# Kernel tuning notes

Measured on AMD Instinct MI355X. Metric: run time of the kernel, lower is better.

The kernel has to match this reference:

```python
import jax, jax.numpy as jnp
import numpy as np

H, NH, NKV, D, I, T, B = 4096, 32, 8, 128, 12288, 1024, 128
THETA, EPS = 1e6, 1e-6


def setup_inputs() -> dict:
    ks = iter(jax.random.split(jax.random.key(0), 64))

    def randn(s):
        return jax.random.normal(next(ks), s, jnp.float32)

    def qw(o, i):
        return jax.random.randint(next(ks), (o, i), 0, 16, jnp.int32)

    def sc(o, g):
        return jax.random.uniform(next(ks), (o, g), jnp.float32, 0.005, 0.02)

    def rot(g):  # block-diagonal rotation, one 128x128 block per input group
        return randn((g, B, B)) / np.float32(np.sqrt(B))

    return dict(
        positions=jnp.arange(T, dtype=jnp.int32),
        hidden_states=randn((T, H)),
        residual=randn((T, H)),
        w_in=jnp.ones(H, jnp.float32), w_post=jnp.ones(H, jnp.float32),
        w_qn=jnp.ones(D, jnp.float32), w_kn=jnp.ones(D, jnp.float32),
        R_q=rot(H // B), qw_q=qw(NH * D, H), sc_q=sc(NH * D, H // B),
        R_k=rot(H // B), qw_k=qw(NKV * D, H), sc_k=sc(NKV * D, H // B),
        R_v=rot(H // B), qw_v=qw(NKV * D, H), sc_v=sc(NKV * D, H // B),
        R_o=rot(NH * D // B), qw_o=qw(H, NH * D), sc_o=sc(H, NH * D // B),
        R_g=rot(H // B), qw_g=qw(I, H), sc_g=sc(I, H // B),
        R_u=rot(H // B), qw_u=qw(I, H), sc_u=sc(I, H // B),
        R_d=rot(I // B), qw_d=qw(H, I), sc_d=sc(H, I // B),
    )


def _rmsnorm(x, w):
    return x * jax.lax.rsqrt(jnp.mean(x * x, -1, keepdims=True) + EPS) * w


def _rot_lin(x, R, qw, sc):
    # RotateLinearInt4: block-rotate input, then int4 group-dequant GEMM.
    G = R.shape[0]
    xr = jnp.einsum('tgi,gij->tgj', x.reshape(-1, G, B), R).reshape(x.shape)
    O = qw.shape[0]
    W = ((qw.astype(x.dtype) - 8.0).reshape(O, G, B) * sc[:, :, None]).reshape(O, G * B)
    return xr @ W.T


def _rope(pos, x):  # neox-style rope, x: [T, h, D]
    half = D // 2
    inv = jnp.power(jnp.float32(THETA), -(jnp.arange(half, dtype=jnp.float32) * (2.0 / D)))
    f = pos.astype(jnp.float32)[:, None] * inv  # [T, half]
    cos, sin = jnp.cos(f)[:, None, :], jnp.sin(f)[:, None, :]
    x1, x2 = x[..., :half], x[..., half:]
    return jnp.concatenate([x1 * cos - x2 * sin, x2 * cos + x1 * sin], -1)


def _forward(positions, hidden_states, residual, w_in, w_post, w_qn, w_kn,
             R_q, qw_q, sc_q, R_k, qw_k, sc_k, R_v, qw_v, sc_v,
             R_o, qw_o, sc_o, R_g, qw_g, sc_g, R_u, qw_u, sc_u,
             R_d, qw_d, sc_d):
    res = hidden_states + residual            # fused add+RMSNorm path
    x = _rmsnorm(res, w_in)
    q = _rot_lin(x, R_q, qw_q, sc_q).reshape(T, NH, D)
    k = _rot_lin(x, R_k, qw_k, sc_k).reshape(T, NKV, D)
    v = _rot_lin(x, R_v, qw_v, sc_v).reshape(T, NKV, D)
    q = _rmsnorm(q, w_qn)                     # per-head q/k RMSNorm
    k = _rmsnorm(k, w_kn)
    q = _rope(positions, q)
    k = _rope(positions, k)
    rep = NH // NKV                           # GQA: repeat kv heads
    kk = jnp.repeat(k, rep, axis=1)
    vv = jnp.repeat(v, rep, axis=1)
    scores = jnp.einsum('thd,shd->hts', q, kk) * (D ** -0.5)
    mask = jnp.tril(jnp.ones((T, T), bool))
    scores = jnp.where(mask, scores, jnp.finfo(scores.dtype).min)
    probs = jax.nn.softmax(scores, -1)
    attn = jnp.einsum('hts,shd->thd', probs, vv).reshape(T, NH * D)
    h = _rot_lin(attn, R_o, qw_o, sc_o)
    res2 = h + res
    x2 = _rmsnorm(res2, w_post)
    gate = _rot_lin(x2, R_g, qw_g, sc_g)
    up = _rot_lin(x2, R_u, qw_u, sc_u)
    h2 = _rot_lin(jax.nn.silu(gate) * up, R_d, qw_d, sc_d)
    return h2, res2


def reference(positions, hidden_states, residual, w_in, w_post, w_qn, w_kn,
              R_q, qw_q, sc_q, R_k, qw_k, sc_k, R_v, qw_v, sc_v,
              R_o, qw_o, sc_o, R_g, qw_g, sc_g, R_u, qw_u, sc_u,
              R_d, qw_d, sc_d):
    return _forward(positions, hidden_states, residual, w_in, w_post, w_qn, w_kn,
                    R_q, qw_q, sc_q, R_k, qw_k, sc_k, R_v, qw_v, sc_v,
                    R_o, qw_o, sc_o, R_g, qw_g, sc_g, R_u, qw_u, sc_u,
                    R_d, qw_d, sc_d)
```

## Files before the change

kernel.cpp:

```cpp
#include <hip/hip_runtime.h>

typedef unsigned short u16;
typedef __attribute__((ext_vector_type(4))) float   f32x4;
typedef __attribute__((ext_vector_type(8))) __bf16  bf16x8;
typedef __attribute__((ext_vector_type(4))) __bf16  bf16x4;
typedef __attribute__((ext_vector_type(8))) short   short8;
typedef __attribute__((ext_vector_type(4))) int     int32x4;
typedef __attribute__((ext_vector_type(4))) short   short4v;

#define MFMA16(a,b,c) __builtin_amdgcn_mfma_f32_16x16x32_bf16(a,b,c,0,0,0)

static __device__ __forceinline__ u16 f2bf(float f){
  unsigned u = __builtin_bit_cast(unsigned, f);
  return (u16)((u + 0x7fffu + ((u >> 16) & 1u)) >> 16);
}
static __device__ __forceinline__ float bf2f(u16 h){
  return __builtin_bit_cast(float, ((unsigned)h) << 16);
}
static __device__ __forceinline__ bf16x8 ldb16(const u16* p){
  return __builtin_bit_cast(bf16x8, *(const short8*)p);
}
static __device__ __forceinline__ void gload_lds16(const void* g, void* l){
  __builtin_amdgcn_global_load_lds(
      reinterpret_cast<const __attribute__((address_space(1))) unsigned int*>(
          reinterpret_cast<unsigned long long>(g)),
      reinterpret_cast<__attribute__((address_space(3))) unsigned int*>(
          reinterpret_cast<unsigned long long>(l)),
      16, 0, 0);
}

static constexpr int T_ = 1024, H_ = 4096, NH_ = 32, NKV_ = 8, I_ = 12288;

__global__ __launch_bounds__(256) void addnorm_kernel(
    const float* __restrict__ a, const float* __restrict__ b,
    const float* __restrict__ w, float* __restrict__ res_out,
    u16* __restrict__ x_out)
{
  const int t = blockIdx.x, tid = threadIdx.x;
  __shared__ float red[4];
  float vals[16]; float ss = 0.f;
  const size_t base = (size_t)t * H_;
  #pragma unroll
  for (int i = 0; i < 16; ++i){
    int c = tid + i*256;
    float v = a[base + c];
    if (b) v += b[base + c];
    vals[i] = v; ss += v*v;
  }
  #pragma unroll
  for (int off = 32; off; off >>= 1) ss += __shfl_xor(ss, off);
  if ((tid & 63) == 0) red[tid >> 6] = ss;
  __syncthreads();
  float tot = red[0] + red[1] + red[2] + red[3];
  float rn = rsqrtf(tot / (float)H_ + 1e-6f);
  #pragma unroll
  for (int i = 0; i < 16; ++i){
    int c = tid + i*256;
    if (res_out) res_out[base + c] = vals[i];
    x_out[base + c] = f2bf(vals[i] * rn * w[c]);
  }
}

__global__ __launch_bounds__(256) void addnorm_red_kernel(
    const float* __restrict__ P, int nsplit,
    const float* __restrict__ resd, const float* __restrict__ w,
    float* __restrict__ res_out, u16* __restrict__ x_out)
{
  const int t = blockIdx.x, tid = threadIdx.x;
  __shared__ float red[4];
  float vals[16]; float ss = 0.f;
  const size_t base = (size_t)t * H_;
  const size_t stride = (size_t)T_ * H_;
  #pragma unroll
  for (int i = 0; i < 16; ++i){
    int c = tid + i*256;
    float v = resd[base + c];
    for (int z = 0; z < nsplit; ++z) v += P[(size_t)z*stride + base + c];
    vals[i] = v; ss += v*v;
  }
  #pragma unroll
  for (int off = 32; off; off >>= 1) ss += __shfl_xor(ss, off);
  if ((tid & 63) == 0) red[tid >> 6] = ss;
  __syncthreads();
  float tot = red[0] + red[1] + red[2] + red[3];
  float rn = rsqrtf(tot / (float)H_ + 1e-6f);
  #pragma unroll
  for (int i = 0; i < 16; ++i){
    int c = tid + i*256;
    res_out[base + c] = vals[i];
    x_out[base + c] = f2bf(vals[i] * rn * w[c]);
  }
}

__global__ __launch_bounds__(256) void rprep_kernel(
    const float* __restrict__ Rq, const float* __restrict__ Rk,
    const float* __restrict__ Rv, const float* __restrict__ Ro,
    const float* __restrict__ Rg_, const float* __restrict__ Ru,
    const float* __restrict__ Rd, u16* __restrict__ Rt)
{
  __shared__ float sR[128][129];
  const int b = blockIdx.x, tid = threadIdx.x;
  const float* src;
  if      (b <  32) src = Rq  + (size_t)(b      ) * 16384;
  else if (b <  64) src = Rk  + (size_t)(b -  32) * 16384;
  else if (b <  96) src = Rv  + (size_t)(b -  64) * 16384;
  else if (b < 128) src = Ro  + (size_t)(b -  96) * 16384;
  else if (b < 160) src = Rg_ + (size_t)(b - 128) * 16384;
  else if (b < 192) src = Ru  + (size_t)(b - 160) * 16384;
  else              src = Rd  + (size_t)(b - 192) * 16384;
  #pragma unroll
  for (int it = 0; it < 16; ++it){
    int idx = (it*256 + tid) * 4;
    float4 v = *(const float4*)&src[idx];
    int i = idx >> 7, j = idx & 127;
    sR[i][j] = v.x; sR[i][j+1] = v.y; sR[i][j+2] = v.z; sR[i][j+3] = v.w;
  }
  __syncthreads();
  u16* dst = Rt + (size_t)b * 16384;
  #pragma unroll
  for (int it = 0; it < 32; ++it){
    int idx = it*256 + tid;
    int j = idx >> 6, i2 = (idx & 63) * 2;
    unsigned lo = f2bf(sR[i2][j]), hi = f2bf(sR[i2+1][j]);
    *(unsigned*)&dst[j*128 + i2] = lo | (hi << 16);
  }
}

__global__ __launch_bounds__(256) void rot_kernel(
    const u16* __restrict__ X, const u16* __restrict__ Rt,
    u16* __restrict__ Y0, u16* __restrict__ Y1, u16* __restrict__ Y2,
    int LD, int gpt, const u16* __restrict__ X2)
{
  __shared__ u16 sX[64][136];
  __shared__ u16 sRt[128][136];
  const int by = blockIdx.y, g = by % gpt;
  const int m0 = blockIdx.x * 64, tid = threadIdx.x;
  u16* Y = (by < gpt) ? Y0 : (by < 2*gpt ? Y1 : Y2);
  #pragma unroll
  for (int i = 0; i < 4; ++i){
    int vid = i*256 + tid, r = vid >> 4, c = (vid & 15) * 8;
    size_t gaddr = (size_t)(m0 + r) * LD + g*128 + c;
    short8 vx = *(const short8*)&X[gaddr];
    if (X2){
      short8 vu = *(const short8*)&X2[gaddr];
      const u16* px = (const u16*)&vx;
      const u16* pu = (const u16*)&vu;
      short8 o;
      u16* po = (u16*)&o;
      #pragma unroll
      for (int e = 0; e < 8; ++e){
        float gv = bf2f(px[e]), uv = bf2f(pu[e]);
        po[e] = f2bf(gv / (1.f + __expf(-gv)) * uv);
      }
      *(short8*)&sX[r][c] = o;
    } else {
      *(short8*)&sX[r][c] = vx;
    }
  }
  const u16* Rg = Rt + (size_t)by * 16384;
  #pragma unroll
  for (int it = 0; it < 8; ++it){
    int idx = it*256 + tid;
    int j = idx >> 4, c8 = (idx & 15) * 8;
    *(short8*)&sRt[j][c8] = *(const short8*)&Rg[j*128 + c8];
  }
  __syncthreads();
  const int lane = tid & 63, w = tid >> 6;
  const int fr = lane & 15, fq = lane >> 4, nw = w * 32;
  f32x4 acc[4][2];
  #pragma unroll
  for (int mi=0;mi<4;mi++)
    #pragma unroll
    for (int ni=0;ni<2;ni++) acc[mi][ni] = (f32x4){0.f,0.f,0.f,0.f};
  #pragma unroll
  for (int kk = 0; kk < 128; kk += 32){
    bf16x8 af[4], bv[2];
    #pragma unroll
    for (int mi=0;mi<4;mi++) af[mi] = ldb16(&sX[mi*16 + fr][kk + fq*8]);
    #pragma unroll
    for (int ni=0;ni<2;ni++) bv[ni] = ldb16(&sRt[nw + ni*16 + fr][kk + fq*8]);
    #pragma unroll
    for (int mi=0;mi<4;mi++)
      #pragma unroll
      for (int ni=0;ni<2;ni++)
        acc[mi][ni] = MFMA16(af[mi], bv[ni], acc[mi][ni]);
  }
  #pragma unroll
  for (int mi=0;mi<4;mi++)
    #pragma unroll
    for (int ni=0;ni<2;ni++)
      #pragma unroll
      for (int rg=0;rg<4;rg++){
        int m = m0 + mi*16 + fq*4 + rg;
        int n = g*128 + nw + ni*16 + fr;
        Y[(size_t)m * LD + n] = f2bf(acc[mi][ni][rg]);
      }
}

template<int NF, bool PARTIAL, bool OUT_BF16>
__global__ __launch_bounds__(512, 1) void gemm_deq(
    const u16* __restrict__ A, const int* __restrict__ QW,
    const float* __restrict__ SC, void* __restrict__ Cout,
    int N, int K, int kc, int nN)
{
  __shared__ u16 sA[2][16384];
  __shared__ u16 sB[2][NF * 4096];
  const int tid = threadIdx.x;
  const int lane = tid & 63, w = tid >> 6;
  const int nblk = gridDim.x, q8 = nblk >> 3, b = blockIdx.x;
  const int l = (b & 7) * q8 + (b >> 3);
  const int mt = l & 3, rest = l >> 2;
  const int nt = rest % nN, z = rest / nN;
  const int bm0 = mt * 256, bn0 = nt * (NF * 64);
  const int kbase = z * kc;
  const int KG = K >> 7;
  const int nkt = kc >> 6;

  f32x4 acc[8][NF];
  #pragma unroll
  for (int i=0;i<8;i++)
    #pragma unroll
    for (int j=0;j<NF;j++) acc[i][j] = (f32x4){0.f,0.f,0.f,0.f};

  const int wr = (w >> 2) * 128, wc = (w & 3) * (NF * 16);
  const int fr = lane & 15, fq = lane >> 4;

  const int l8 = lane >> 3;
  const size_t K2 = (size_t)K * 2;
  const char* gA0 = (const char*)A
      + ((size_t)(bm0 + w*32 + l8) * K + (size_t)kbase) * 2
      + (((lane & 7) * 16) ^ (l8 << 4));
  auto ADMA = [&](int kt, int c){
    const char* g = gA0 + (size_t)kt * 128;
    char* lb = (char*)&sA[c][0] + (w*32) * 128;
    #pragma unroll
    for (int i=0;i<4;i++)
      gload_lds16(g + (size_t)(i*8) * K2, lb + i*1024);
  };

  const int rBr = tid >> 4, cB4 = (tid & 15) * 4;
  const int* gB0 = QW + (size_t)(bn0 + rBr) * K + kbase + cB4;
  const float* gS0 = SC + (size_t)(bn0 + rBr) * KG;
  const int sBx = (cB4 * 2) ^ ((rBr & 7) << 4);

  int32x4 rB[2*NF];
  float   rS[2*NF];
  auto loadB = [&](int kt){
    const int* gb = gB0 + kt*64;
    const int g = (kbase + kt*64) >> 7;
    const float* ps = gS0 + g;
    #pragma unroll
    for (int i=0;i<2*NF;i++){
      rB[i] = *(const int32x4*)(gb + (size_t)i*32*K);
      rS[i] = ps[(size_t)i*32*KG];
    }
  };
  auto storeB = [&](int c){
    #pragma unroll
    for (int i=0;i<2*NF;i++){
      float s = rS[i], ns = -8.f * s;
      bf16x4 o;
      o[0] = (__bf16)fmaf((float)rB[i].x, s, ns);
      o[1] = (__bf16)fmaf((float)rB[i].y, s, ns);
      o[2] = (__bf16)fmaf((float)rB[i].z, s, ns);
      o[3] = (__bf16)fmaf((float)rB[i].w, s, ns);
      *(bf16x4*)((char*)&sB[c][0] + (rBr + 32*i)*128 + sBx) = o;
    }
  };

  auto mfma_half = [&](int c, int kk){
    bf16x8 af[8], bv[NF];
    #pragma unroll
    for (int mi=0;mi<8;mi++){
      int r = wr + mi*16 + fr;
      af[mi] = *(const bf16x8*)((const char*)&sA[c][0] + r*128 +
                ((kk*64 + fq*16) ^ ((r & 7) << 4)));
    }
    #pragma unroll
    for (int ni=0;ni<NF;ni++){
      int r = wc + ni*16 + fr;
      bv[ni] = *(const bf16x8*)((const char*)&sB[c][0] + r*128 +
                ((kk*64 + fq*16) ^ ((r & 7) << 4)));
    }
    __builtin_amdgcn_s_setprio(1);
    #pragma unroll
    for (int mi=0;mi<8;mi++)
      #pragma unroll
      for (int ni=0;ni<NF;ni++)
        acc[mi][ni] = MFMA16(af[mi], bv[ni], acc[mi][ni]);
    __builtin_amdgcn_s_setprio(0);
  };

#define WAIT_ADMA() do { if (NF==3) asm volatile("s_waitcnt vmcnt(12)" ::: "memory"); \
                         else       asm volatile("s_waitcnt vmcnt(16)" ::: "memory"); } while(0)

  loadB(0);
  ADMA(0, 0);
  asm volatile("s_waitcnt vmcnt(4)" ::: "memory");
  __builtin_amdgcn_sched_barrier(0);
  storeB(0);
  if (nkt > 1){ loadB(1); __builtin_amdgcn_sched_barrier(0); }
  WAIT_ADMA();
  asm volatile("s_waitcnt lgkmcnt(0)" ::: "memory");
  __builtin_amdgcn_s_barrier();

  int cb = 0;
  for (int t = 0; t < nkt; ++t){
    const bool more  = (t + 1) < nkt;
    const bool more2 = (t + 2) < nkt;
    if (more){
      ADMA(t+1, cb ^ 1);
      __builtin_amdgcn_sched_barrier(0);
    }
    mfma_half(cb, 0);
    if (more){
      asm volatile("s_waitcnt vmcnt(4)" ::: "memory");
      __builtin_amdgcn_sched_barrier(0);
      storeB(cb ^ 1);
      __builtin_amdgcn_sched_barrier(0);
    }
    mfma_half(cb, 1);
    if (more){
      if (more2){
        loadB(t+2);
        __builtin_amdgcn_sched_barrier(0);
        WAIT_ADMA();
      } else {
        asm volatile("s_waitcnt vmcnt(0)" ::: "memory");
      }
      asm volatile("s_waitcnt lgkmcnt(0)" ::: "memory");
      __builtin_amdgcn_sched_barrier(0);
      __builtin_amdgcn_s_barrier();
      cb ^= 1;
    }
  }
#undef WAIT_ADMA

  #pragma unroll
  for (int mi=0;mi<8;mi++)
    #pragma unroll
    for (int ni=0;ni<NF;ni++)
      #pragma unroll
      for (int rg=0;rg<4;rg++){
        size_t m = bm0 + wr + mi*16 + fq*4 + rg;
        size_t n = bn0 + wc + ni*16 + fr;
        float v = acc[mi][ni][rg];
        if (PARTIAL)          ((float*)Cout)[((size_t)z*1024 + m) * N + n] = v;
        else if (OUT_BF16)    ((u16*)Cout)[m * N + n] = f2bf(v);
        else                  ((float*)Cout)[m * N + n] = v;
      }
}

__global__ __launch_bounds__(256) void reduce_splits(
    const float* __restrict__ P, int nsplit, int n,
    const float* __restrict__ addend, float* __restrict__ outf, u16* __restrict__ outb)
{
  size_t base = ((size_t)blockIdx.x*256 + threadIdx.x) * 4;
  if (base >= (size_t)n) return;
  f32x4 s = *(const f32x4*)&P[base];
  for (int j = 1; j < nsplit; ++j)
    s += *(const f32x4*)&P[(size_t)j*n + base];
  if (addend) s += *(const f32x4*)&addend[base];
  if (outb){
    short4v o;
    #pragma unroll
    for (int e=0;e<4;e++) o[e] = (short)f2bf(s[e]);
    *(short4v*)&outb[base] = o;
  } else {
    *(f32x4*)&outf[base] = s;
  }
}

__global__ __launch_bounds__(64) void qknorm_rope_red(
    const float* __restrict__ P, int nsplit, int nh,
    const float* __restrict__ w, const int* __restrict__ pos, u16* __restrict__ out)
{
  const int t = blockIdx.x, h = blockIdx.y, j = threadIdx.x;
  const int N = nh * 128;
  const size_t stride = (size_t)T_ * N;
  const size_t base = (size_t)t * N + h*128;
  float x1 = 0.f, x2 = 0.f;
  for (int z = 0; z < nsplit; ++z){
    x1 += P[(size_t)z*stride + base + j];
    x2 += P[(size_t)z*stride + base + j + 64];
  }
  float ss = x1*x1 + x2*x2;
  #pragma unroll
  for (int off = 32; off; off >>= 1) ss += __shfl_xor(ss, off);
  float rn = rsqrtf(ss / 128.f + 1e-6f);
  float xn1 = x1 * rn * w[j], xn2 = x2 * rn * w[j + 64];
  float inv = exp2f(-(float)j * (19.93156856932417f / 64.f));
  float f = (float)pos[t] * inv;
  float sv, cv; sincosf(f, &sv, &cv);
  u16* orow = out + ((size_t)t * nh + h) * 128;
  orow[j]      = f2bf(xn1 * cv - xn2 * sv);
  orow[j + 64] = f2bf(xn2 * cv + xn1 * sv);
}

__global__ __launch_bounds__(256) void attn_kernel(
    const u16* __restrict__ Q, const u16* __restrict__ Kc,
    const u16* __restrict__ Vc, u16* __restrict__ O)
{
  __shared__ u16 sK[32][136];
  __shared__ u16 sVt[128][40];
  __shared__ u16 sP[4][16][40];
  const int b = blockIdx.x;
  const int qt = (b < 256) ? (b & 15) : (15 - (b & 15));
  const int h = b >> 4;
  const int kvh = h >> 2;
  const int tid = threadIdx.x, lane = tid & 63, w = tid >> 6;
  const int fr = lane & 15, fq = lane >> 4;
  const int r0 = qt*64 + w*16;
  const float scale = 0.08838834764831845f;
  bf16x8 aq[4];
  #pragma unroll
  for (int kd=0;kd<4;kd++)
    aq[kd] = ldb16(&Q[(size_t)(r0 + fr) * 4096 + h*128 + kd*32 + fq*8]);
  f32x4 accO[8];
  #pragma unroll
  for (int ni=0;ni<8;ni++) accO[ni] = (f32x4){0.f,0.f,0.f,0.f};
  float mrow[4] = {-1e30f,-1e30f,-1e30f,-1e30f};
  float lrow[4] = {0.f,0.f,0.f,0.f};
  const int ntiles = (qt + 1) * 2;
  for (int jt = 0; jt < ntiles; ++jt){
    __syncthreads();
    #pragma unroll
    for (int i=0;i<2;i++){
      int vid = i*256 + tid, r = vid >> 4, c = (vid & 15) * 8;
      *(short8*)&sK[r][c] = *(const short8*)&Kc[(size_t)(jt*32 + r) * 1024 + kvh*128 + c];
      short8 vv = *(const short8*)&Vc[(size_t)(jt*32 + r) * 1024 + kvh*128 + c];
      const u16* pv = (const u16*)&vv;
      #pragma unroll
      for (int e=0;e<8;e++) sVt[c + e][r] = pv[e];
    }
    __syncthreads();
    f32x4 accS[2]; accS[0] = (f32x4){0.f,0.f,0.f,0.f}; accS[1] = accS[0];
    #pragma unroll
    for (int kd=0;kd<4;kd++){
      #pragma unroll
      for (int ni=0;ni<2;ni++){
        bf16x8 bk = ldb16(&sK[ni*16 + fr][kd*32 + fq*8]);
        accS[ni] = MFMA16(aq[kd], bk, accS[ni]);
      }
    }
    float s[2][4];
    #pragma unroll
    for (int ni=0;ni<2;ni++)
      #pragma unroll
      for (int rg=0;rg<4;rg++){
        int row = r0 + fq*4 + rg, col = jt*32 + ni*16 + fr;
        float v = accS[ni][rg] * scale;
        s[ni][rg] = (col <= row) ? v : -1e30f;
      }
    float alpha[4];
    #pragma unroll
    for (int rg=0;rg<4;rg++){
      float mx = fmaxf(s[0][rg], s[1][rg]);
      #pragma unroll
      for (int off=1; off<16; off<<=1) mx = fmaxf(mx, __shfl_xor(mx, off, 16));
      float mnew = fmaxf(mrow[rg], mx);
      alpha[rg] = __expf(mrow[rg] - mnew);
      mrow[rg] = mnew;
      float p0 = __expf(s[0][rg] - mnew), p1 = __expf(s[1][rg] - mnew);
      s[0][rg] = p0; s[1][rg] = p1;
      float ps = p0 + p1;
      #pragma unroll
      for (int off=1; off<16; off<<=1) ps += __shfl_xor(ps, off, 16);
      lrow[rg] = lrow[rg] * alpha[rg] + ps;
    }
    #pragma unroll
    for (int ni=0;ni<2;ni++)
      #pragma unroll
      for (int rg=0;rg<4;rg++)
        sP[w][fq*4 + rg][ni*16 + fr] = f2bf(s[ni][rg]);
    __syncthreads();
    #pragma unroll
    for (int ni=0;ni<8;ni++)
      #pragma unroll
      for (int rg=0;rg<4;rg++) accO[ni][rg] *= alpha[rg];
    bf16x8 ap = ldb16(&sP[w][fr][fq*8]);
    #pragma unroll
    for (int ni=0;ni<8;ni++){
      bf16x8 bv = ldb16(&sVt[ni*16 + fr][fq*8]);
      accO[ni] = MFMA16(ap, bv, accO[ni]);
    }
  }
  #pragma unroll
  for (int ni=0;ni<8;ni++)
    #pragma unroll
    for (int rg=0;rg<4;rg++){
      int row = r0 + fq*4 + rg, col = h*128 + ni*16 + fr;
      O[(size_t)row * 4096 + col] = f2bf(accO[ni][rg] / lrow[rg]);
    }
}

extern "C" void kernel_launch(void* const* d_in, const int* in_sizes, int n_in,
                              void* d_out, int out_size, void* d_ws, size_t ws_size,
                              hipStream_t stream)
{
  const int*   positions = (const int*)  d_in[0];
  const float* hs    = (const float*)d_in[1];
  const float* resid = (const float*)d_in[2];
  const float* w_in  = (const float*)d_in[3];
  const float* w_post= (const float*)d_in[4];
  const float* w_qn  = (const float*)d_in[5];
  const float* w_kn  = (const float*)d_in[6];
  const float* R_q = (const float*)d_in[7];
  const int*   qw_q= (const int*)  d_in[8];
  const float* sc_q= (const float*)d_in[9];
  const float* R_k = (const float*)d_in[10];
  const int*   qw_k= (const int*)  d_in[11];
  const float* sc_k= (const float*)d_in[12];
  const float* R_v = (const float*)d_in[13];
  const int*   qw_v= (const int*)  d_in[14];
  const float* sc_v= (const float*)d_in[15];
  const float* R_o = (const float*)d_in[16];
  const int*   qw_o= (const int*)  d_in[17];
  const float* sc_o= (const float*)d_in[18];
  const float* R_g = (const float*)d_in[19];
  const int*   qw_g= (const int*)  d_in[20];
  const float* sc_g= (const float*)d_in[21];
  const float* R_u = (const float*)d_in[22];
  const int*   qw_u= (const int*)  d_in[23];
  const float* sc_u= (const float*)d_in[24];
  const float* R_d = (const float*)d_in[25];
  const int*   qw_d= (const int*)  d_in[26];
  const float* sc_d= (const float*)d_in[27];
  (void)in_sizes; (void)n_in; (void)out_size; (void)ws_size;

  char* wsp = (char*)d_ws; size_t off = 0;
  auto alloc = [&](size_t bytes)->void*{
    void* p = wsp + off; off += (bytes + 255) & ~(size_t)255; return p;
  };
  float* res  = (float*)alloc((size_t)T_*H_*4);
  u16*   xbf  = (u16*)  alloc((size_t)T_*H_*2);
  u16*   xrA  = (u16*)  alloc((size_t)T_*H_*2);
  u16*   xrB  = (u16*)  alloc((size_t)T_*H_*2);
  u16*   xrC  = (u16*)  alloc((size_t)T_*H_*2);
  float* qf   = (float*)alloc((size_t)T_*4096*4);
  float* kf   = (float*)alloc((size_t)T_*1024*4);
  u16*   qbf  = (u16*)  alloc((size_t)T_*4096*2);
  u16*   kbf  = (u16*)  alloc((size_t)T_*1024*2);
  u16*   vbf  = (u16*)  alloc((size_t)T_*1024*2);
  u16*   abf  = (u16*)  alloc((size_t)T_*4096*2);
  u16*   gbf  = (u16*)  alloc((size_t)T_*I_*2);
  u16*   ubf  = (u16*)  alloc((size_t)T_*I_*2);
  u16*   hbf  = (u16*)  alloc((size_t)T_*I_*2);
  u16*   Rtb  = (u16*)  alloc((size_t)288*16384*2);
  (void)qf; (void)kf;

  float* pQKV = (float*)gbf;
  float* pO   = (float*)gbf;
  float* pD   = (float*)wsp;

  float* h2   = (float*)d_out;
  float* res2 = (float*)d_out + (size_t)T_*H_;

  rprep_kernel<<<288, 256, 0, stream>>>(R_q, R_k, R_v, R_o, R_g, R_u, R_d, Rtb);
  addnorm_kernel<<<T_, 256, 0, stream>>>(hs, resid, w_in, res, xbf);
  rot_kernel<<<dim3(16,96),256,0,stream>>>(xbf, Rtb, xrA, xrB, xrC, H_, 32, nullptr);
  gemm_deq<4,true ,false><<<256,512,0,stream>>>(xrA, qw_q, sc_q, pQKV, 4096, 4096, 1024, 16);
  qknorm_rope_red<<<dim3(T_,NH_ ),64,0,stream>>>(pQKV, 4, NH_, w_qn, positions, qbf);
  gemm_deq<4,true ,false><<<256,512,0,stream>>>(xrB, qw_k, sc_k, pQKV, 1024, 4096, 256, 4);
  qknorm_rope_red<<<dim3(T_,NKV_),64,0,stream>>>(pQKV, 16, NKV_, w_kn, positions, kbf);
  gemm_deq<4,true ,false><<<256,512,0,stream>>>(xrC, qw_v, sc_v, pQKV, 1024, 4096, 256, 4);
  reduce_splits<<<(T_*1024)/1024,256,0,stream>>>(pQKV, 16, T_*1024, nullptr, nullptr, vbf);
  attn_kernel<<<512,256,0,stream>>>(qbf, kbf, vbf, abf);
  rot_kernel<<<dim3(16,32),256,0,stream>>>(abf, Rtb + (size_t)96*16384, xrA, nullptr, nullptr, H_, 32, nullptr);
  gemm_deq<4,true ,false><<<256,512,0,stream>>>(xrA, qw_o, sc_o, pO, 4096, 4096, 1024, 16);
  addnorm_red_kernel<<<T_,256,0,stream>>>(pO, 4, res, w_post, res2, xbf);
  rot_kernel<<<dim3(16,64),256,0,stream>>>(xbf, Rtb + (size_t)128*16384, xrA, xrB, nullptr, H_, 32, nullptr);
  gemm_deq<3,false,true ><<<256,512,0,stream>>>(xrA, qw_g, sc_g, gbf, 12288, 4096, 4096, 64);
  gemm_deq<3,false,true ><<<256,512,0,stream>>>(xrB, qw_u, sc_u, ubf, 12288, 4096, 4096, 64);
  rot_kernel<<<dim3(16,96),256,0,stream>>>(gbf, Rtb + (size_t)192*16384, hbf, nullptr, nullptr, I_, 96, ubf);
  gemm_deq<4,true ,false><<<256,512,0,stream>>>(hbf, qw_d, sc_d, pD, 4096, 12288, 3072, 16);
  reduce_splits<<<(T_*4096)/1024,256,0,stream>>>(pD, 4, T_*4096, nullptr, h2, nullptr);
}
```

Measured before the change: 809.2 us.

## Halve gemm_deq M tile and K step, double grid for occupancy

The dequant GEMM now uses a 128-row M tile instead of 256 and a 32-wide K step instead of 64, with all shared-memory layouts, swizzles, loader indexing and wait counts rewritten to match. Each block uses far less LDS and fewer accumulators, the launch-bounds minimum-occupancy hint is dropped, and every GEMM launch goes to 512 blocks so more blocks can sit on each CU. In exchange, the dequantized weight tiles are reused across fewer activation rows, which means more weight loading and more dequant work overall. The shorter K step also brings more barriers per unit of work and a smaller MFMA batch between syncs.

```diff
diff --git a/kernel.cpp b/kernel.cpp
--- a/kernel.cpp
+++ b/kernel.cpp
@@ -198,109 +198,104 @@
 }
 
 template<int NF, bool PARTIAL, bool OUT_BF16>
-__global__ __launch_bounds__(512, 1) void gemm_deq(
+__global__ __launch_bounds__(512) void gemm_deq(
     const u16* __restrict__ A, const int* __restrict__ QW,
     const float* __restrict__ SC, void* __restrict__ Cout,
     int N, int K, int kc, int nN)
 {
-  __shared__ u16 sA[2][16384];
-  __shared__ u16 sB[2][NF * 4096];
+  __shared__ u16 sA[2][4096];
+  __shared__ u16 sB[2][NF * 2048];
   const int tid = threadIdx.x;
   const int lane = tid & 63, w = tid >> 6;
   const int nblk = gridDim.x, q8 = nblk >> 3, b = blockIdx.x;
   const int l = (b & 7) * q8 + (b >> 3);
-  const int mt = l & 3, rest = l >> 2;
+  const int mt = l & 7, rest = l >> 3;
   const int nt = rest % nN, z = rest / nN;
-  const int bm0 = mt * 256, bn0 = nt * (NF * 64);
+  const int bm0 = mt * 128, bn0 = nt * (NF * 64);
   const int kbase = z * kc;
   const int KG = K >> 7;
-  const int nkt = kc >> 6;
-
-  f32x4 acc[8][NF];
-  #pragma unroll
-  for (int i=0;i<8;i++)
+  const int nkt = kc >> 5;
+
+  f32x4 acc[4][NF];
+  #pragma unroll
+  for (int i=0;i<4;i++)
     #pragma unroll
     for (int j=0;j<NF;j++) acc[i][j] = (f32x4){0.f,0.f,0.f,0.f};
 
-  const int wr = (w >> 2) * 128, wc = (w & 3) * (NF * 16);
+  const int wr = (w >> 2) * 64, wc = (w & 3) * (NF * 16);
   const int fr = lane & 15, fq = lane >> 4;
 
-  const int l8 = lane >> 3;
-  const size_t K2 = (size_t)K * 2;
+  const int lr = lane >> 2;
   const char* gA0 = (const char*)A
-      + ((size_t)(bm0 + w*32 + l8) * K + (size_t)kbase) * 2
-      + (((lane & 7) * 16) ^ (l8 << 4));
+      + ((size_t)(bm0 + w*16 + lr) * K + (size_t)kbase) * 2
+      + (((lane & 3) * 16) ^ ((lr & 3) << 4));
   auto ADMA = [&](int kt, int c){
-    const char* g = gA0 + (size_t)kt * 128;
-    char* lb = (char*)&sA[c][0] + (w*32) * 128;
-    #pragma unroll
-    for (int i=0;i<4;i++)
-      gload_lds16(g + (size_t)(i*8) * K2, lb + i*1024);
+    gload_lds16(gA0 + (size_t)kt * 64, (char*)&sA[c][0] + w * 1024);
   };
 
-  const int rBr = tid >> 4, cB4 = (tid & 15) * 4;
-  const int* gB0 = QW + (size_t)(bn0 + rBr) * K + kbase + cB4;
-  const float* gS0 = SC + (size_t)(bn0 + rBr) * KG;
-  const int sBx = (cB4 * 2) ^ ((rBr & 7) << 4);
-
-  int32x4 rB[2*NF];
-  float   rS[2*NF];
+  const int rB0 = tid >> 3, cB = (tid & 7) * 4;
+  const int* gB0 = QW + (size_t)(bn0 + rB0) * K + kbase + cB;
+  const float* gS0 = SC + (size_t)(bn0 + rB0) * KG;
+  const int sBx = (cB * 2) ^ ((rB0 & 3) << 4);
+
+  int32x4 rB[NF];
+  float   rS[NF];
   auto loadB = [&](int kt){
-    const int* gb = gB0 + kt*64;
-    const int g = (kbase + kt*64) >> 7;
+    const int* gb = gB0 + kt*32;
+    const int g = (kbase + kt*32) >> 7;
     const float* ps = gS0 + g;
     #pragma unroll
-    for (int i=0;i<2*NF;i++){
-      rB[i] = *(const int32x4*)(gb + (size_t)i*32*K);
-      rS[i] = ps[(size_t)i*32*KG];
+    for (int i=0;i<NF;i++){
+      rB[i] = *(const int32x4*)(gb + (size_t)i*64*K);
+      rS[i] = ps[(size_t)i*64*KG];
     }
   };
   auto storeB = [&](int c){
     #pragma unroll
-    for (int i=0;i<2*NF;i++){
+    for (int i=0;i<NF;i++){
       float s = rS[i], ns = -8.f * s;
       bf16x4 o;
       o[0] = (__bf16)fmaf((float)rB[i].x, s, ns);
       o[1] = (__bf16)fmaf((float)rB[i].y, s, ns);
       o[2] = (__bf16)fmaf((float)rB[i].z, s, ns);
       o[3] = (__bf16)fmaf((float)rB[i].w, s, ns);
-      *(bf16x4*)((char*)&sB[c][0] + (rBr + 32*i)*128 + sBx) = o;
+      *(bf16x4*)((char*)&sB[c][0] + (rB0 + 64*i)*64 + sBx) = o;
     }
   };
 
-  auto mfma_half = [&](int c, int kk){
-    bf16x8 af[8], bv[NF];
-    #pragma unroll
-    for (int mi=0;mi<8;mi++){
+  auto mfma_tile = [&](int c){
+    bf16x8 af[4], bv[NF];
+    #pragma unroll
+    for (int mi=0;mi<4;mi++){
       int r = wr + mi*16 + fr;
-      af[mi] = *(const bf16x8*)((const char*)&sA[c][0] + r*128 +
-                ((kk*64 + fq*16) ^ ((r & 7) << 4)));
+      af[mi] = *(const bf16x8*)((const char*)&sA[c][0] + r*64 +
+                ((fq*16) ^ ((r & 3) << 4)));
     }
     #pragma unroll
     for (int ni=0;ni<NF;ni++){
       int r = wc + ni*16 + fr;
-      bv[ni] = *(const bf16x8*)((const char*)&sB[c][0] + r*128 +
-                ((kk*64 + fq*16) ^ ((r & 7) << 4)));
+      bv[ni] = *(const bf16x8*)((const char*)&sB[c][0] + r*64 +
+                ((fq*16) ^ ((r & 3) << 4)));
     }
     __builtin_amdgcn_s_setprio(1);
     #pragma unroll
-    for (int mi=0;mi<8;mi++)
+    for (int mi=0;mi<4;mi++)
       #pragma unroll
       for (int ni=0;ni<NF;ni++)
         acc[mi][ni] = MFMA16(af[mi], bv[ni], acc[mi][ni]);
     __builtin_amdgcn_s_setprio(0);
   };
 
-#define WAIT_ADMA() do { if (NF==3) asm volatile("s_waitcnt vmcnt(12)" ::: "memory"); \
-                         else       asm volatile("s_waitcnt vmcnt(16)" ::: "memory"); } while(0)
+#define WAIT_2NF() do { if (NF==3) asm volatile("s_waitcnt vmcnt(6)" ::: "memory"); \
+                        else       asm volatile("s_waitcnt vmcnt(8)" ::: "memory"); } while(0)
 
   loadB(0);
   ADMA(0, 0);
-  asm volatile("s_waitcnt vmcnt(4)" ::: "memory");
+  asm volatile("s_waitcnt vmcnt(1)" ::: "memory");
   __builtin_amdgcn_sched_barrier(0);
   storeB(0);
   if (nkt > 1){ loadB(1); __builtin_amdgcn_sched_barrier(0); }
-  WAIT_ADMA();
+  WAIT_2NF();
   asm volatile("s_waitcnt lgkmcnt(0)" ::: "memory");
   __builtin_amdgcn_s_barrier();
 
@@ -312,19 +307,16 @@
       ADMA(t+1, cb ^ 1);
       __builtin_amdgcn_sched_barrier(0);
     }
-    mfma_half(cb, 0);
+    mfma_tile(cb);
     if (more){
-      asm volatile("s_waitcnt vmcnt(4)" ::: "memory");
+      asm volatile("s_waitcnt vmcnt(1)" ::: "memory");
       __builtin_amdgcn_sched_barrier(0);
       storeB(cb ^ 1);
       __builtin_amdgcn_sched_barrier(0);
-    }
-    mfma_half(cb, 1);
-    if (more){
       if (more2){
         loadB(t+2);
         __builtin_amdgcn_sched_barrier(0);
-        WAIT_ADMA();
+        WAIT_2NF();
       } else {
         asm volatile("s_waitcnt vmcnt(0)" ::: "memory");
       }
@@ -334,10 +326,10 @@
       cb ^= 1;
     }
   }
-#undef WAIT_ADMA
-
-  #pragma unroll
-  for (int mi=0;mi<8;mi++)
+#undef WAIT_2NF
+
+  #pragma unroll
+  for (int mi=0;mi<4;mi++)
     #pragma unroll
     for (int ni=0;ni<NF;ni++)
       #pragma unroll
@@ -559,20 +551,20 @@
   rprep_kernel<<<288, 256, 0, stream>>>(R_q, R_k, R_v, R_o, R_g, R_u, R_d, Rtb);
   addnorm_kernel<<<T_, 256, 0, stream>>>(hs, resid, w_in, res, xbf);
   rot_kernel<<<dim3(16,96),256,0,stream>>>(xbf, Rtb, xrA, xrB, xrC, H_, 32, nullptr);
-  gemm_deq<4,true ,false><<<256,512,0,stream>>>(xrA, qw_q, sc_q, pQKV, 4096, 4096, 1024, 16);
+  gemm_deq<4,true ,false><<<512,512,0,stream>>>(xrA, qw_q, sc_q, pQKV, 4096, 4096, 1024, 16);
   qknorm_rope_red<<<dim3(T_,NH_ ),64,0,stream>>>(pQKV, 4, NH_, w_qn, positions, qbf);
-  gemm_deq<4,true ,false><<<256,512,0,stream>>>(xrB, qw_k, sc_k, pQKV, 1024, 4096, 256, 4);
+  gemm_deq<4,true ,false><<<512,512,0,stream>>>(xrB, qw_k, sc_k, pQKV, 1024, 4096, 256, 4);
   qknorm_rope_red<<<dim3(T_,NKV_),64,0,stream>>>(pQKV, 16, NKV_, w_kn, positions, kbf);
-  gemm_deq<4,true ,false><<<256,512,0,stream>>>(xrC, qw_v, sc_v, pQKV, 1024, 4096, 256, 4);
+  gemm_deq<4,true ,false><<<512,512,0,stream>>>(xrC, qw_v, sc_v, pQKV, 1024, 4096, 256, 4);
   reduce_splits<<<(T_*1024)/1024,256,0,stream>>>(pQKV, 16, T_*1024, nullptr, nullptr, vbf);
   attn_kernel<<<512,256,0,stream>>>(qbf, kbf, vbf, abf);
   rot_kernel<<<dim3(16,32),256,0,stream>>>(abf, Rtb + (size_t)96*16384, xrA, nullptr, nullptr, H_, 32, nullptr);
-  gemm_deq<4,true ,false><<<256,512,0,stream>>>(xrA, qw_o, sc_o, pO, 4096, 4096, 1024, 16);
+  gemm_deq<4,true ,false><<<512,512,0,stream>>>(xrA, qw_o, sc_o, pO, 4096, 4096, 1024, 16);
   addnorm_red_kernel<<<T_,256,0,stream>>>(pO, 4, res, w_post, res2, xbf);
   rot_kernel<<<dim3(16,64),256,0,stream>>>(xbf, Rtb + (size_t)128*16384, xrA, xrB, nullptr, H_, 32, nullptr);
-  gemm_deq<3,false,true ><<<256,512,0,stream>>>(xrA, qw_g, sc_g, gbf, 12288, 4096, 4096, 64);
-  gemm_deq<3,false,true ><<<256,512,0,stream>>>(xrB, qw_u, sc_u, ubf, 12288, 4096, 4096, 64);
+  gemm_deq<3,false,true ><<<512,512,0,stream>>>(xrA, qw_g, sc_g, gbf, 12288, 4096, 4096, 64);
+  gemm_deq<3,false,true ><<<512,512,0,stream>>>(xrB, qw_u, sc_u, ubf, 12288, 4096, 4096, 64);
   rot_kernel<<<dim3(16,96),256,0,stream>>>(gbf, Rtb + (size_t)192*16384, hbf, nullptr, nullptr, I_, 96, ubf);
-  gemm_deq<4,true ,false><<<256,512,0,stream>>>(hbf, qw_d, sc_d, pD, 4096, 12288, 3072, 16);
+  gemm_deq<4,true ,false><<<512,512,0,stream>>>(hbf, qw_d, sc_d, pD, 4096, 12288, 3072, 16);
   reduce_splits<<<(T_*4096)/1024,256,0,stream>>>(pD, 4, T_*4096, nullptr, h2, nullptr);
 }
```

Measured after the change: 1.207 ms. 1.49x slower.

## Warp-specialize dequant GEMM into producer and MFMA consumer waves

Applied to the files above, without the earlier changes.

The dequant GEMM now launches 768 threads: 8 consumer waves only read LDS and issue MFMAs, while 4 producer waves load the A tile via global-to-LDS DMA, load int4 weights and scales, dequantize them, and write them into the double-buffered LDS. The aim is to stop consumer waves from stalling on global loads and dequant arithmetic, so matrix-core issue runs continuously. In exchange it adds waves per CU and more per-thread register pressure in the producers. Producer and consumer paths must now match their barrier counts exactly, and the producers wait on vmcnt(0) every iteration, which may serialize their loads.

```diff
diff --git a/kernel.cpp b/kernel.cpp
--- a/kernel.cpp
+++ b/kernel.cpp
@@ -198,7 +198,7 @@
 }
 
 template<int NF, bool PARTIAL, bool OUT_BF16>
-__global__ __launch_bounds__(512, 1) void gemm_deq(
+__global__ __launch_bounds__(768, 1) void gemm_deq(
     const u16* __restrict__ A, const int* __restrict__ QW,
     const float* __restrict__ SC, void* __restrict__ Cout,
     int N, int K, int kc, int nN)
@@ -216,139 +216,156 @@
   const int KG = K >> 7;
   const int nkt = kc >> 6;
 
-  f32x4 acc[8][NF];
-  #pragma unroll
-  for (int i=0;i<8;i++)
-    #pragma unroll
-    for (int j=0;j<NF;j++) acc[i][j] = (f32x4){0.f,0.f,0.f,0.f};
-
-  const int wr = (w >> 2) * 128, wc = (w & 3) * (NF * 16);
-  const int fr = lane & 15, fq = lane >> 4;
-
-  const int l8 = lane >> 3;
-  const size_t K2 = (size_t)K * 2;
-  const char* gA0 = (const char*)A
-      + ((size_t)(bm0 + w*32 + l8) * K + (size_t)kbase) * 2
-      + (((lane & 7) * 16) ^ (l8 << 4));
-  auto ADMA = [&](int kt, int c){
-    const char* g = gA0 + (size_t)kt * 128;
-    char* lb = (char*)&sA[c][0] + (w*32) * 128;
-    #pragma unroll
-    for (int i=0;i<4;i++)
-      gload_lds16(g + (size_t)(i*8) * K2, lb + i*1024);
-  };
-
-  const int rBr = tid >> 4, cB4 = (tid & 15) * 4;
-  const int* gB0 = QW + (size_t)(bn0 + rBr) * K + kbase + cB4;
-  const float* gS0 = SC + (size_t)(bn0 + rBr) * KG;
-  const int sBx = (cB4 * 2) ^ ((rBr & 7) << 4);
-
-  int32x4 rB[2*NF];
-  float   rS[2*NF];
-  auto loadB = [&](int kt){
-    const int* gb = gB0 + kt*64;
-    const int g = (kbase + kt*64) >> 7;
-    const float* ps = gS0 + g;
-    #pragma unroll
-    for (int i=0;i<2*NF;i++){
-      rB[i] = *(const int32x4*)(gb + (size_t)i*32*K);
-      rS[i] = ps[(size_t)i*32*KG];
-    }
-  };
-  auto storeB = [&](int c){
-    #pragma unroll
-    for (int i=0;i<2*NF;i++){
-      float s = rS[i], ns = -8.f * s;
-      bf16x4 o;
-      o[0] = (__bf16)fmaf((float)rB[i].x, s, ns);
-      o[1] = (__bf16)fmaf((float)rB[i].y, s, ns);
-      o[2] = (__bf16)fmaf((float)rB[i].z, s, ns);
-      o[3] = (__bf16)fmaf((float)rB[i].w, s, ns);
-      *(bf16x4*)((char*)&sB[c][0] + (rBr + 32*i)*128 + sBx) = o;
-    }
-  };
-
-  auto mfma_half = [&](int c, int kk){
-    bf16x8 af[8], bv[NF];
-    #pragma unroll
-    for (int mi=0;mi<8;mi++){
-      int r = wr + mi*16 + fr;
-      af[mi] = *(const bf16x8*)((const char*)&sA[c][0] + r*128 +
-                ((kk*64 + fq*16) ^ ((r & 7) << 4)));
-    }
-    #pragma unroll
-    for (int ni=0;ni<NF;ni++){
-      int r = wc + ni*16 + fr;
-      bv[ni] = *(const bf16x8*)((const char*)&sB[c][0] + r*128 +
-                ((kk*64 + fq*16) ^ ((r & 7) << 4)));
-    }
-    __builtin_amdgcn_s_setprio(1);
-    #pragma unroll
-    for (int mi=0;mi<8;mi++)
-      #pragma unroll
-      for (int ni=0;ni<NF;ni++)
-        acc[mi][ni] = MFMA16(af[mi], bv[ni], acc[mi][ni]);
-    __builtin_amdgcn_s_setprio(0);
-  };
-
-#define WAIT_ADMA() do { if (NF==3) asm volatile("s_waitcnt vmcnt(12)" ::: "memory"); \
-                         else       asm volatile("s_waitcnt vmcnt(16)" ::: "memory"); } while(0)
-
-  loadB(0);
-  ADMA(0, 0);
-  asm volatile("s_waitcnt vmcnt(4)" ::: "memory");
-  __builtin_amdgcn_sched_barrier(0);
-  storeB(0);
-  if (nkt > 1){ loadB(1); __builtin_amdgcn_sched_barrier(0); }
-  WAIT_ADMA();
-  asm volatile("s_waitcnt lgkmcnt(0)" ::: "memory");
-  __builtin_amdgcn_s_barrier();
-
-  int cb = 0;
-  for (int t = 0; t < nkt; ++t){
-    const bool more  = (t + 1) < nkt;
-    const bool more2 = (t + 2) < nkt;
-    if (more){
-      ADMA(t+1, cb ^ 1);
-      __builtin_amdgcn_sched_barrier(0);
-    }
-    mfma_half(cb, 0);
-    if (more){
-      asm volatile("s_waitcnt vmcnt(4)" ::: "memory");
-      __builtin_amdgcn_sched_barrier(0);
-      storeB(cb ^ 1);
-      __builtin_amdgcn_sched_barrier(0);
-    }
-    mfma_half(cb, 1);
-    if (more){
-      if (more2){
-        loadB(t+2);
-        __builtin_amdgcn_sched_barrier(0);
-        WAIT_ADMA();
-      } else {
-        asm volatile("s_waitcnt vmcnt(0)" ::: "memory");
-      }
-      asm volatile("s_waitcnt lgkmcnt(0)" ::: "memory");
-      __builtin_amdgcn_sched_barrier(0);
+  if (w < 8){
+    f32x4 acc[8][NF];
+    #pragma unroll
+    for (int i=0;i<8;i++)
+      #pragma unroll
+      for (int j=0;j<NF;j++) acc[i][j] = (f32x4){0.f,0.f,0.f,0.f};
+    const int wr = (w >> 2) * 128, wc = (w & 3) * (NF * 16);
+    const int fr = lane & 15, fq = lane >> 4;
+
+    __builtin_amdgcn_s_barrier();
+
+    int cb = 0;
+    for (int t = 0; t < nkt; ++t){
+      #pragma unroll
+      for (int kk = 0; kk < 2; ++kk){
+        bf16x8 af[8], bv[NF];
+        #pragma unroll
+        for (int mi=0;mi<8;mi++){
+          int r = wr + mi*16 + fr;
+          af[mi] = *(const bf16x8*)((const char*)&sA[cb][0] + r*128 +
+                    ((kk*64 + fq*16) ^ ((r & 7) << 4)));
+        }
+        #pragma unroll
+        for (int ni=0;ni<NF;ni++){
+          int r = wc + ni*16 + fr;
+          bv[ni] = *(const bf16x8*)((const char*)&sB[cb][0] + r*128 +
+                    ((kk*64 + fq*16) ^ ((r & 7) << 4)));
+        }
+        __builtin_amdgcn_s_setprio(1);
+        #pragma unroll
+        for (int mi=0;mi<8;mi++)
+          #pragma unroll
+          for (int ni=0;ni<NF;ni++)
+            acc[mi][ni] = MFMA16(af[mi], bv[ni], acc[mi][ni]);
+        __builtin_amdgcn_s_setprio(0);
+      }
       __builtin_amdgcn_s_barrier();
       cb ^= 1;
     }
-  }
-#undef WAIT_ADMA
-
-  #pragma unroll
-  for (int mi=0;mi<8;mi++)
-    #pragma unroll
-    for (int ni=0;ni<NF;ni++)
-      #pragma unroll
-      for (int rg=0;rg<4;rg++){
-        size_t m = bm0 + wr + mi*16 + fq*4 + rg;
-        size_t n = bn0 + wc + ni*16 + fr;
-        float v = acc[mi][ni][rg];
-        if (PARTIAL)          ((float*)Cout)[((size_t)z*1024 + m) * N + n] = v;
-        else if (OUT_BF16)    ((u16*)Cout)[m * N + n] = f2bf(v);
-        else                  ((float*)Cout)[m * N + n] = v;
-      }
+
+    #pragma unroll
+    for (int mi=0;mi<8;mi++)
+      #pragma unroll
+      for (int ni=0;ni<NF;ni++)
+        #pragma unroll
+        for (int rg=0;rg<4;rg++){
+          size_t m = bm0 + wr + mi*16 + fq*4 + rg;
+          size_t n = bn0 + wc + ni*16 + fr;
+          float v = acc[mi][ni][rg];
+          if (PARTIAL)          ((float*)Cout)[((size_t)z*1024 + m) * N + n] = v;
+          else if (OUT_BF16)    ((u16*)Cout)[m * N + n] = f2bf(v);
+          else                  ((float*)Cout)[m * N + n] = v;
+        }
+  } else {
+    const int t2 = tid - 512;
+    const int pw = w - 8;
+    const int l8 = lane >> 3;
+    const size_t K2 = (size_t)K * 2;
+    const char* gA0 = (const char*)A
+        + ((size_t)(bm0 + pw*64 + l8) * K + (size_t)kbase) * 2
+        + (((lane & 7) * 16) ^ (l8 << 4));
+    auto ADMA = [&](int kt, int c){
+      const char* g = gA0 + (size_t)kt * 128;
+      char* lb = (char*)&sA[c][0] + (pw*64) * 128;
+      #pragma unroll
+      for (int i=0;i<8;i++)
+        gload_lds16(g + (size_t)(i*8) * K2, lb + i*1024);
+    };
+    const int rp = t2 >> 2, ci = (t2 & 3) * 16;
+    const int* gB0 = QW + (size_t)(bn0 + rp) * K + kbase + ci;
+    const float* gS0 = SC + (size_t)(bn0 + rp) * KG;
+
+    int32x4 rX[NF*4], rY[NF*4];
+    float   sX[NF],  sY[NF];
+    auto loadB = [&](int kt, int32x4 (&rB)[NF*4], float (&rS)[NF]){
+      const int* gb = gB0 + kt*64;
+      const int g = (kbase + kt*64) >> 7;
+      const float* ps = gS0 + g;
+      #pragma unroll
+      for (int i=0;i<NF;i++){
+        #pragma unroll
+        for (int j=0;j<4;j++)
+          rB[i*4+j] = *(const int32x4*)(gb + (size_t)i*64*K + j*4);
+        rS[i] = ps[(size_t)i*64*KG];
+      }
+    };
+    auto storeB = [&](int c, int32x4 (&rB)[NF*4], float (&rS)[NF]){
+      #pragma unroll
+      for (int i=0;i<NF;i++){
+        float s = rS[i], ns = -8.f * s;
+        const int row = rp + 64*i;
+        #pragma unroll
+        for (int jh=0;jh<2;jh++){
+          bf16x8 o;
+          #pragma unroll
+          for (int j=0;j<2;j++){
+            int32x4 q = rB[i*4 + jh*2 + j];
+            o[j*4+0] = (__bf16)fmaf((float)q.x, s, ns);
+            o[j*4+1] = (__bf16)fmaf((float)q.y, s, ns);
+            o[j*4+2] = (__bf16)fmaf((float)q.z, s, ns);
+            o[j*4+3] = (__bf16)fmaf((float)q.w, s, ns);
+          }
+          *(bf16x8*)((char*)&sB[c][0] + row*128 +
+                     (((ci + jh*8) * 2) ^ ((row & 7) << 4))) = o;
+        }
+      }
+    };
+
+#define P_RETIRE_B()    asm volatile("s_waitcnt vmcnt(8)" ::: "memory")
+#define P_RETIRE_ADMA() do { if (NF==3) asm volatile("s_waitcnt vmcnt(15)" ::: "memory"); \
+                             else       asm volatile("s_waitcnt vmcnt(20)" ::: "memory"); } while(0)
+
+    loadB(0, rX, sX);
+    ADMA(0, 0);
+    P_RETIRE_B();
+    __builtin_amdgcn_sched_barrier(0);
+    storeB(0, rX, sX);
+    if (nkt > 1) loadB(1, rY, sY);
+    __builtin_amdgcn_sched_barrier(0);
+    if (nkt > 1) P_RETIRE_ADMA();
+    else         asm volatile("s_waitcnt vmcnt(0)" ::: "memory");
+    asm volatile("s_waitcnt lgkmcnt(0)" ::: "memory");
+    __builtin_amdgcn_s_barrier();
+
+    int cb = 0;
+    for (int t = 0; t < nkt; ++t){
+      const bool m1 = (t+1) < nkt, m2 = (t+2) < nkt;
+      if (m1){
+        asm volatile("s_waitcnt vmcnt(0)" ::: "memory");
+        __builtin_amdgcn_sched_barrier(0);
+        if (t & 1){
+          storeB(cb ^ 1, rX, sX);
+          ADMA(t+1, cb ^ 1);
+          if (m2) loadB(t+2, rY, sY);
+        } else {
+          storeB(cb ^ 1, rY, sY);
+          ADMA(t+1, cb ^ 1);
+          if (m2) loadB(t+2, rX, sX);
+        }
+        __builtin_amdgcn_sched_barrier(0);
+        if (m2) P_RETIRE_ADMA();
+        else    asm volatile("s_waitcnt vmcnt(0)" ::: "memory");
+        asm volatile("s_waitcnt lgkmcnt(0)" ::: "memory");
+      }
+      __builtin_amdgcn_s_barrier();
+      cb ^= 1;
+    }
+#undef P_RETIRE_B
+#undef P_RETIRE_ADMA
+  }
 }
 
 __global__ __launch_bounds__(256) void reduce_splits(
@@ -559,20 +576,20 @@
   rprep_kernel<<<288, 256, 0, stream>>>(R_q, R_k, R_v, R_o, R_g, R_u, R_d, Rtb);
   addnorm_kernel<<<T_, 256, 0, stream>>>(hs, resid, w_in, res, xbf);
   rot_kernel<<<dim3(16,96),256,0,stream>>>(xbf, Rtb, xrA, xrB, xrC, H_, 32, nullptr);
-  gemm_deq<4,true ,false><<<256,512,0,stream>>>(xrA, qw_q, sc_q, pQKV, 4096, 4096, 1024, 16);
+  gemm_deq<4,true ,false><<<256,768,0,stream>>>(xrA, qw_q, sc_q, pQKV, 4096, 4096, 1024, 16);
   qknorm_rope_red<<<dim3(T_,NH_ ),64,0,stream>>>(pQKV, 4, NH_, w_qn, positions, qbf);
-  gemm_deq<4,true ,false><<<256,512,0,stream>>>(xrB, qw_k, sc_k, pQKV, 1024, 4096, 256, 4);
+  gemm_deq<4,true ,false><<<256,768,0,stream>>>(xrB, qw_k, sc_k, pQKV, 1024, 4096, 256, 4);
   qknorm_rope_red<<<dim3(T_,NKV_),64,0,stream>>>(pQKV, 16, NKV_, w_kn, positions, kbf);
-  gemm_deq<4,true ,false><<<256,512,0,stream>>>(xrC, qw_v, sc_v, pQKV, 1024, 4096, 256, 4);
+  gemm_deq<4,true ,false><<<256,768,0,stream>>>(xrC, qw_v, sc_v, pQKV, 1024, 4096, 256, 4);
   reduce_splits<<<(T_*1024)/1024,256,0,stream>>>(pQKV, 16, T_*1024, nullptr, nullptr, vbf);
   attn_kernel<<<512,256,0,stream>>>(qbf, kbf, vbf, abf);
   rot_kernel<<<dim3(16,32),256,0,stream>>>(abf, Rtb + (size_t)96*16384, xrA, nullptr, nullptr, H_, 32, nullptr);
-  gemm_deq<4,true ,false><<<256,512,0,stream>>>(xrA, qw_o, sc_o, pO, 4096, 4096, 1024, 16);
+  gemm_deq<4,true ,false><<<256,768,0,stream>>>(xrA, qw_o, sc_o, pO, 4096, 4096, 1024, 16);
   addnorm_red_kernel<<<T_,256,0,stream>>>(pO, 4, res, w_post, res2, xbf);
   rot_kernel<<<dim3(16,64),256,0,stream>>>(xbf, Rtb + (size_t)128*16384, xrA, xrB, nullptr, H_, 32, nullptr);
-  gemm_deq<3,false,true ><<<256,512,0,stream>>>(xrA, qw_g, sc_g, gbf, 12288, 4096, 4096, 64);
-  gemm_deq<3,false,true ><<<256,512,0,stream>>>(xrB, qw_u, sc_u, ubf, 12288, 4096, 4096, 64);
+  gemm_deq<3,false,true ><<<256,768,0,stream>>>(xrA, qw_g, sc_g, gbf, 12288, 4096, 4096, 64);
+  gemm_deq<3,false,true ><<<256,768,0,stream>>>(xrB, qw_u, sc_u, ubf, 12288, 4096, 4096, 64);
   rot_kernel<<<dim3(16,96),256,0,stream>>>(gbf, Rtb + (size_t)192*16384, hbf, nullptr, nullptr, I_, 96, ubf);
-  gemm_deq<4,true ,false><<<256,512,0,stream>>>(hbf, qw_d, sc_d, pD, 4096, 12288, 3072, 16);
+  gemm_deq<4,true ,false><<<256,768,0,stream>>>(hbf, qw_d, sc_d, pD, 4096, 12288, 3072, 16);
   reduce_splits<<<(T_*4096)/1024,256,0,stream>>>(pD, 4, T_*4096, nullptr, h2, nullptr);
 }
```

Result: slower. 1.623 ms (+100.5%).
